# Kernel tuning notes

Hardware: AMD Instinct MI355X
Metric: run time of the kernel (lower is better)

## Reference

```python
import jax, jax.numpy as jnp
import numpy as np

N_USERS = 100000
N_ITEMS = 200000
N_NODES = N_USERS + N_ITEMS
EMB_DIM = 64
N_LAYERS = 3
NNZ = 4000000


def setup_inputs() -> dict:
    key = jax.random.key(0)
    k1, k2, k3, k4, k5 = jax.random.split(key, 5)
    # xavier_uniform bound for [n, d] embedding
    bu = float(np.sqrt(6.0 / (N_USERS + EMB_DIM)))
    bi = float(np.sqrt(6.0 / (N_ITEMS + EMB_DIM)))
    user_table = jax.random.uniform(k1, (N_USERS, EMB_DIM), jnp.float32, -bu, bu)
    item_table = jax.random.uniform(k2, (N_ITEMS, EMB_DIM), jnp.float32, -bi, bi)
    adj_rows = jax.random.randint(k3, (NNZ,), 0, N_NODES, dtype=jnp.int32)
    adj_cols = jax.random.randint(k4, (NNZ,), 0, N_NODES, dtype=jnp.int32)
    # symmetric-normalized adjacency values are small positive floats
    adj_vals = jax.random.uniform(k5, (NNZ,), jnp.float32) * 0.1
    return {"user_table": user_table, "item_table": item_table,
            "adj_rows": adj_rows, "adj_cols": adj_cols, "adj_vals": adj_vals}


def _spmm(rows, cols, vals, x):
    # out[r] = sum_{nnz with row r} vals * x[col]  (COO SpMM)
    msgs = vals[:, None] * x[cols]                      # [nnz, D]
    return jax.ops.segment_sum(msgs, rows, num_segments=N_NODES)


def reference(user_table, item_table, adj_rows, adj_cols, adj_vals):
    # forward(adj_norm, perturb=False) in eval mode (dropout inactive)
    emb = jnp.concatenate([user_table, item_table], axis=0)  # [N, D]
    acc = emb  # running sum over layer outputs (incl. layer 0)
    cur = emb
    for _ in range(N_LAYERS):
        cur = _spmm(adj_rows, adj_cols, adj_vals, cur)
        acc = acc + cur
    all_emb = acc / (N_LAYERS + 1)  # mean over stacked layer embeddings
    user_emb = all_emb[:N_USERS]
    item_emb = all_emb[N_USERS:]
    return (user_emb, item_emb)
```

## Files before the change

kernel.cpp:

```cpp
#include <hip/hip_runtime.h>

#define N_USERS 100000
#define N_ITEMS 200000
#define N_NODES (N_USERS + N_ITEMS)
#define EMB     64
#define NNZ     4000000

#define BSHIFT 10
#define BROWS  (1 << BSHIFT)
#define NBUCK  ((N_NODES + BROWS - 1) >> BSHIFT)

#define AGG_THR    512
#define AGG_EPT    8
#define AGG_T      (AGG_THR * AGG_EPT)
#define AGG_BLOCKS ((NNZ + AGG_T - 1) / AGG_T)
#define SCAN_N     512

#define SEGCAP 16384
#define PCAP   SEGCAP
#define PITER  (PCAP / 1024)

typedef _Float16 h4 __attribute__((ext_vector_type(4)));


__global__ __launch_bounds__(AGG_THR)
void bucket_agg_kernel(const int*   __restrict__ rows,
                       const int*   __restrict__ cols,
                       const float* __restrict__ vals,
                       int*         __restrict__ bcnt,
                       float2*      __restrict__ pay) {
    __shared__ int            cntS[SCAN_N];
    __shared__ int            hoff[SCAN_N];
    __shared__ float2         payS[AGG_T];
    __shared__ unsigned short bidS[AGG_T];

    int tid  = threadIdx.x;
    int base = blockIdx.x * AGG_T;

    for (int i = tid; i < SCAN_N; i += AGG_THR) cntS[i] = 0;
    __syncthreads();

    unsigned pk[AGG_EPT];
#pragma unroll
    for (int j = 0; j < AGG_EPT; j++) {
        int e = base + j * AGG_THR + tid;
        pk[j] = 0xFFFFFFFFu;
        if (e < NNZ) {
            int r  = rows[e];
            int b  = r >> BSHIFT;
            int lp = atomicAdd(&cntS[b], 1);
            pk[j]  = ((unsigned)b << 22) | ((unsigned)(r & (BROWS - 1)) << 12)
                   | (unsigned)lp;
        }
    }
    __syncthreads();

    int v = cntS[tid];
    for (int off = 1; off < SCAN_N; off <<= 1) {
        int t = 0;
        if (tid >= off) t = cntS[tid - off];
        __syncthreads();
        if (tid >= off) cntS[tid] += t;
        __syncthreads();
    }
    int excl = cntS[tid] - v;

    if (tid < NBUCK && v > 0) hoff[tid] = atomicAdd(&bcnt[tid * 16], v);
    __syncthreads();
    cntS[tid] = excl;
    __syncthreads();

#pragma unroll
    for (int j = 0; j < AGG_EPT; j++) {
        if (pk[j] != 0xFFFFFFFFu) {
            int e   = base + j * AGG_THR + tid;
            int b   = pk[j] >> 22;
            int rl  = (pk[j] >> 12) & (BROWS - 1);
            int lp  = pk[j] & 0xFFF;
            int idx = cntS[b] + lp;
            unsigned packed = (unsigned)cols[e] | ((unsigned)rl << 19);
            payS[idx] = make_float2(__uint_as_float(packed), vals[e]);
            bidS[idx] = (unsigned short)b;
        }
    }
    __syncthreads();

    int total = NNZ - base; if (total > AGG_T) total = AGG_T;
    for (int i = tid; i < total; i += AGG_THR) {
        int b   = bidS[i];
        int pos = hoff[b] + (i - cntS[b]);
        if (pos < SEGCAP)
            pay[(size_t)b * SEGCAP + pos] = payS[i];
    }
}

__global__ void bscan_kernel(const int* __restrict__ bcnt,
                             int* __restrict__ bbase,
                             int* __restrict__ row_ptr) {
    __shared__ int s[512];
    int tid = threadIdx.x;
    int v = 0;
    if (tid < NBUCK) {
        v = bcnt[tid * 16];
        if (v > SEGCAP) v = SEGCAP;
    }
    s[tid] = v;
    __syncthreads();
    for (int off = 1; off < 512; off <<= 1) {
        int t = 0;
        if (tid >= off) t = s[tid - off];
        __syncthreads();
        if (tid >= off) s[tid] += t;
        __syncthreads();
    }
    if (tid < NBUCK) bbase[tid] = s[tid] - v;
    if (tid == 511) bbase[NBUCK] = s[511];
    if (tid == 0)   row_ptr[N_NODES] = NNZ;
}

__global__ __launch_bounds__(1024)
void place_kernel(const int*    __restrict__ bcnt,
                  const int*    __restrict__ bbase,
                  const float2* __restrict__ pay,
                  int*          __restrict__ row_ptr,
                  float2*       __restrict__ edges) {
    __shared__ float2 payS[PCAP];
    __shared__ int    cntS[BROWS];
    int b   = blockIdx.x;
    int tid = threadIdx.x;
    int run = bcnt[b * 16]; if (run > PCAP) run = PCAP;
    int beg = bbase[b];
    const float2* seg = pay + (size_t)b * SEGCAP;

    cntS[tid] = 0;
    __syncthreads();

    unsigned eu[PITER]; float ev[PITER]; int elp[PITER];
#pragma unroll
    for (int j = 0; j < PITER; j++) {
        int i = j * 1024 + tid;
        eu[j] = 0xFFFFFFFFu;
        if (i < run) {
            float2 p = seg[i];
            unsigned u = __float_as_uint(p.x);
            eu[j] = u;
            ev[j] = p.y;
            elp[j] = atomicAdd(&cntS[(u >> 19) & (BROWS - 1)], 1);
        }
    }
    __syncthreads();

    for (int off = 1; off < BROWS; off <<= 1) {
        int t = 0;
        if (tid >= off) t = cntS[tid - off];
        __syncthreads();
        if (tid >= off) cntS[tid] += t;
        __syncthreads();
    }

    int gr = (b << BSHIFT) + tid;
    if (gr < N_NODES)
        row_ptr[gr] = beg + (tid ? cntS[tid - 1] : 0);

#pragma unroll
    for (int j = 0; j < PITER; j++) {
        if (eu[j] != 0xFFFFFFFFu) {
            int r    = (int)((eu[j] >> 19) & (BROWS - 1));
            int base = (r == 0) ? 0 : cntS[r - 1];
            payS[base + elp[j]] = make_float2(__uint_as_float(eu[j] & 0x7FFFFu), ev[j]);
        }
    }
    __syncthreads();

    for (int i = tid; i < run; i += 1024) {
        edges[beg + i] = payS[i];
    }
}

__global__ void initH_kernel(const float* __restrict__ user_t,
                             const float* __restrict__ item_t,
                             _Float16* __restrict__ eh) {
    int i = blockIdx.x * blockDim.x + threadIdx.x;
    const int total4 = N_NODES * EMB / 4;
    if (i >= total4) return;
    int fi   = i * 4;
    int node = fi >> 6;
    int off  = fi & 63;
    float4 v;
    if (node < N_USERS)
        v = *(const float4*)(user_t + (size_t)node * EMB + off);
    else
        v = *(const float4*)(item_t + (size_t)(node - N_USERS) * EMB + off);
    h4 h = { (_Float16)v.x, (_Float16)v.y, (_Float16)v.z, (_Float16)v.w };
    *(h4*)(eh + fi) = h;
}

__device__ __forceinline__ float4 row_gather_h(const int*      __restrict__ rp,
                                               const float2*   __restrict__ edges,
                                               const _Float16* __restrict__ xh,
                                               int row, int s) {
    int i   = rp[row];
    int end = rp[row + 1];
    float4 acc = make_float4(0.f, 0.f, 0.f, 0.f);
    for (; i + 3 < end; i += 4) {
        float2 e0 = edges[i];
        float2 e1 = edges[i + 1];
        float2 e2 = edges[i + 2];
        float2 e3 = edges[i + 3];
        h4 a = *(const h4*)(xh + ((size_t)__float_as_int(e0.x) << 6) + (s << 2));
        h4 b = *(const h4*)(xh + ((size_t)__float_as_int(e1.x) << 6) + (s << 2));
        h4 c = *(const h4*)(xh + ((size_t)__float_as_int(e2.x) << 6) + (s << 2));
        h4 d = *(const h4*)(xh + ((size_t)__float_as_int(e3.x) << 6) + (s << 2));
        acc.x += e0.y * (float)a.x + e1.y * (float)b.x + e2.y * (float)c.x + e3.y * (float)d.x;
        acc.y += e0.y * (float)a.y + e1.y * (float)b.y + e2.y * (float)c.y + e3.y * (float)d.y;
        acc.z += e0.y * (float)a.z + e1.y * (float)b.z + e2.y * (float)c.z + e3.y * (float)d.z;
        acc.w += e0.y * (float)a.w + e1.y * (float)b.w + e2.y * (float)c.w + e3.y * (float)d.w;
    }
    for (; i < end; ++i) {
        float2 e0 = edges[i];
        h4 a = *(const h4*)(xh + ((size_t)__float_as_int(e0.x) << 6) + (s << 2));
        acc.x += e0.y * (float)a.x;
        acc.y += e0.y * (float)a.y;
        acc.z += e0.y * (float)a.z;
        acc.w += e0.y * (float)a.w;
    }
    return acc;
}

__global__ void spmm_yh_kernel(const int*      __restrict__ rp,
                               const float2*   __restrict__ edges,
                               const _Float16* __restrict__ xh,
                               _Float16*       __restrict__ yh) {
    int t    = blockIdx.x * blockDim.x + threadIdx.x;
    int wid  = t >> 6;
    int lane = t & 63;
    int q    = lane >> 4;
    int s    = lane & 15;
    int row  = (wid << 2) + q;
    if (row >= N_NODES) return;
    float4 acc = row_gather_h(rp, edges, xh, row, s);
    h4 h = { (_Float16)acc.x, (_Float16)acc.y, (_Float16)acc.z, (_Float16)acc.w };
    *(h4*)(yh + (((size_t)row << 6) + (s << 2))) = h;
}

__global__ void spmm_fin_kernel(const int*      __restrict__ rp,
                                const float2*   __restrict__ edges,
                                const float*    __restrict__ user_t,
                                const float*    __restrict__ item_t,
                                const _Float16* __restrict__ y1h,
                                const _Float16* __restrict__ y2h,
                                float*          __restrict__ out) {
    int t    = blockIdx.x * blockDim.x + threadIdx.x;
    int wid  = t >> 6;
    int lane = t & 63;
    int q    = lane >> 4;
    int s    = lane & 15;
    int row  = (wid << 2) + q;
    if (row >= N_NODES) return;
    float4 acc = row_gather_h(rp, edges, y2h, row, s);
    size_t o = ((size_t)row << 6) + (s << 2);
    float4 ev;
    if (row < N_USERS)
        ev = *(const float4*)(user_t + o);
    else
        ev = *(const float4*)(item_t + o - ((size_t)N_USERS << 6));
    h4 v1 = *(const h4*)(y1h + o);
    h4 v2 = *(const h4*)(y2h + o);
    float4 r;
    r.x = (ev.x + (float)v1.x + (float)v2.x + acc.x) * 0.25f;
    r.y = (ev.y + (float)v1.y + (float)v2.y + acc.y) * 0.25f;
    r.z = (ev.z + (float)v1.z + (float)v2.z + acc.z) * 0.25f;
    r.w = (ev.w + (float)v1.w + (float)v2.w + acc.w) * 0.25f;
    *(float4*)(out + o) = r;
}

__global__ void init_kernel(const float* __restrict__ user_t,
                            const float* __restrict__ item_t,
                            float* __restrict__ out,
                            float* __restrict__ bufA,
                            float* __restrict__ bufB) {
    int i = blockIdx.x * blockDim.x + threadIdx.x;
    const int total4 = N_NODES * EMB / 4;
    if (i >= total4) return;
    int fi   = i * 4;
    int node = fi >> 6;
    int off  = fi & 63;
    float4 v;
    if (node < N_USERS)
        v = *(const float4*)(user_t + (size_t)node * EMB + off);
    else
        v = *(const float4*)(item_t + (size_t)(node - N_USERS) * EMB + off);
    *(float4*)(out  + fi) = v;
    *(float4*)(bufA + fi) = v;
    *(float4*)(bufB + fi) = make_float4(0.f, 0.f, 0.f, 0.f);
}

__global__ void spmm_kernel(const int*   __restrict__ rows,
                            const int*   __restrict__ cols,
                            const float* __restrict__ vals,
                            const float* __restrict__ x,
                            float*       __restrict__ y) {
    int tid  = blockIdx.x * blockDim.x + threadIdx.x;
    int e    = tid >> 6;
    int lane = tid & 63;
    if (e >= NNZ) return;
    atomicAdd(&y[(size_t)rows[e] * EMB + lane], vals[e] * x[(size_t)cols[e] * EMB + lane]);
}

__global__ void acc_zero_kernel(float* __restrict__ out,
                                const float* __restrict__ src,
                                float* __restrict__ zbuf) {
    int i = blockIdx.x * blockDim.x + threadIdx.x;
    const int total4 = N_NODES * EMB / 4;
    if (i >= total4) return;
    int fi = i * 4;
    float4 o = *(float4*)(out + fi);
    float4 s = *(const float4*)(src + fi);
    o.x += s.x; o.y += s.y; o.z += s.z; o.w += s.w;
    *(float4*)(out  + fi) = o;
    *(float4*)(zbuf + fi) = make_float4(0.f, 0.f, 0.f, 0.f);
}

__global__ void final_kernel(float* __restrict__ out,
                             const float* __restrict__ src) {
    int i = blockIdx.x * blockDim.x + threadIdx.x;
    const int total4 = N_NODES * EMB / 4;
    if (i >= total4) return;
    int fi = i * 4;
    float4 o = *(float4*)(out + fi);
    float4 s = *(const float4*)(src + fi);
    o.x = (o.x + s.x) * 0.25f;
    o.y = (o.y + s.y) * 0.25f;
    o.z = (o.z + s.z) * 0.25f;
    o.w = (o.w + s.w) * 0.25f;
    *(float4*)(out + fi) = o;
}

extern "C" void kernel_launch(void* const* d_in, const int* in_sizes, int n_in,
                              void* d_out, int out_size, void* d_ws, size_t ws_size,
                              hipStream_t stream) {
    const float* user_t = (const float*)d_in[0];
    const float* item_t = (const float*)d_in[1];
    const int*   rows   = (const int*)d_in[2];
    const int*   cols   = (const int*)d_in[3];
    const float* vals   = (const float*)d_in[4];
    float* out = (float*)d_out;

    const size_t embh_bytes = (size_t)N_NODES * EMB * 2;
    const size_t emb_bytes  = (size_t)N_NODES * EMB * 4;
    const size_t pay_bytes  = (size_t)NBUCK * SEGCAP * 8;
    const size_t r0_bytes   = (pay_bytes > embh_bytes ? pay_bytes : embh_bytes);
    const size_t edges_bytes = (size_t)NNZ * 8;
    const size_t small_bytes = (size_t)(N_NODES + 1) * 4
                             + (size_t)NBUCK * 16 * 4
                             + (size_t)(NBUCK + 1) * 4;
    const int total4    = N_NODES * EMB / 4;
    const int ew_blocks = (total4 + 255) / 256;

    const size_t need_h = r0_bytes + 2 * embh_bytes + edges_bytes + small_bytes;
    const int spmm_blocks = (int)(((size_t)N_NODES / 4 * 64 + 255) / 256);

    if (ws_size >= need_h) {
        char* p = (char*)d_ws;
        char*     region0 = p;           p += r0_bytes;
        _Float16* y1h     = (_Float16*)p; p += embh_bytes;
        _Float16* y2h     = (_Float16*)p; p += embh_bytes;
        float2*   edges   = (float2*)p;   p += edges_bytes;
        int*      row_ptr = (int*)p;      p += (size_t)(N_NODES + 1) * 4;
        int*      bcnt    = (int*)p;      p += (size_t)NBUCK * 16 * 4;
        int*      bbase   = (int*)p;
        float2*   pay = (float2*)region0;
        _Float16* eh  = (_Float16*)region0;

        hipMemsetAsync(bcnt, 0, (size_t)NBUCK * 16 * 4, stream);
        bucket_agg_kernel<<<AGG_BLOCKS, AGG_THR, 0, stream>>>(rows, cols, vals, bcnt, pay);
        bscan_kernel<<<1, 512, 0, stream>>>(bcnt, bbase, row_ptr);
        place_kernel<<<NBUCK, 1024, 0, stream>>>(bcnt, bbase, pay, row_ptr, edges);

        initH_kernel<<<ew_blocks, 256, 0, stream>>>(user_t, item_t, eh);

        spmm_yh_kernel <<<spmm_blocks, 256, 0, stream>>>(row_ptr, edges, eh,  y1h);
        spmm_yh_kernel <<<spmm_blocks, 256, 0, stream>>>(row_ptr, edges, y1h, y2h);
        spmm_fin_kernel<<<spmm_blocks, 256, 0, stream>>>(row_ptr, edges, user_t, item_t,
                                                         y1h, y2h, out);
    } else {
        char* p = (char*)d_ws;
        float* bufA = (float*)p; p += emb_bytes;
        float* bufB = (float*)p;
        const int spmmA_blocks = (int)(((size_t)NNZ * 64 + 255) / 256);
        init_kernel<<<ew_blocks, 256, 0, stream>>>(user_t, item_t, out, bufA, bufB);
        spmm_kernel<<<spmmA_blocks, 256, 0, stream>>>(rows, cols, vals, bufA, bufB);
        acc_zero_kernel<<<ew_blocks, 256, 0, stream>>>(out, bufB, bufA);
        spmm_kernel<<<spmmA_blocks, 256, 0, stream>>>(rows, cols, vals, bufB, bufA);
        acc_zero_kernel<<<ew_blocks, 256, 0, stream>>>(out, bufA, bufB);
        spmm_kernel<<<spmmA_blocks, 256, 0, stream>>>(rows, cols, vals, bufA, bufB);
        final_kernel<<<ew_blocks, 256, 0, stream>>>(out, bufB);
    }
}
```

Measured before the change: 511.6 us.

## Halve bucket size, use wave-shuffle scans, fuse fp16 embedding init into place kernel

Bucket width drops from 1024 to 512 rows, so there are about 586 buckets. The place kernel now runs 512 threads with half the shared memory, which should allow more blocks per CU. The shared-memory Hillis-Steele scans with a barrier per step are replaced by wave shuffle scans plus a cross-wave prefix, which cuts barrier count. The separate fp16 conversion kernel is folded into the place kernel, which removes a launch. In exchange the pay buffer and eh no longer alias, so more workspace is needed. The fused conversion uses scalar loads rather than float4, and the per-bucket capacity is halved to 8192, which would silently drop edges if a bucket overflowed (mean load is about 6.8k per bucket).

```diff
diff --git a/kernel.cpp b/kernel.cpp
--- a/kernel.cpp
+++ b/kernel.cpp
@@ -6,22 +6,30 @@
 #define EMB     64
 #define NNZ     4000000
 
-#define BSHIFT 10
+#define BSHIFT 9
 #define BROWS  (1 << BSHIFT)
 #define NBUCK  ((N_NODES + BROWS - 1) >> BSHIFT)
+#define NB2    1024
 
 #define AGG_THR    512
 #define AGG_EPT    8
 #define AGG_T      (AGG_THR * AGG_EPT)
 #define AGG_BLOCKS ((NNZ + AGG_T - 1) / AGG_T)
-#define SCAN_N     512
-
-#define SEGCAP 16384
-#define PCAP   SEGCAP
-#define PITER  (PCAP / 1024)
+
+#define SEGCAP 8192
+#define PITER  (SEGCAP / 512)
 
 typedef _Float16 h4 __attribute__((ext_vector_type(4)));
 
+
+__device__ __forceinline__ int wave_incl_scan(int v, int lane) {
+#pragma unroll
+    for (int d = 1; d < 64; d <<= 1) {
+        int t = __shfl_up(v, d, 64);
+        if (lane >= d) v += t;
+    }
+    return v;
+}
 
 __global__ __launch_bounds__(AGG_THR)
 void bucket_agg_kernel(const int*   __restrict__ rows,
@@ -29,15 +37,19 @@
                        const float* __restrict__ vals,
                        int*         __restrict__ bcnt,
                        float2*      __restrict__ pay) {
-    __shared__ int            cntS[SCAN_N];
-    __shared__ int            hoff[SCAN_N];
+    __shared__ int            cntS[NB2];
+    __shared__ int            hoff[NB2];
+    __shared__ int            waveTotS[8];
     __shared__ float2         payS[AGG_T];
     __shared__ unsigned short bidS[AGG_T];
 
     int tid  = threadIdx.x;
+    int lane = tid & 63;
+    int wid  = tid >> 6;
     int base = blockIdx.x * AGG_T;
 
-    for (int i = tid; i < SCAN_N; i += AGG_THR) cntS[i] = 0;
+    cntS[tid]       = 0;
+    cntS[tid + 512] = 0;
     __syncthreads();
 
     unsigned pk[AGG_EPT];
@@ -49,32 +61,34 @@
             int r  = rows[e];
             int b  = r >> BSHIFT;
             int lp = atomicAdd(&cntS[b], 1);
-            pk[j]  = ((unsigned)b << 22) | ((unsigned)(r & (BROWS - 1)) << 12)
+            pk[j]  = ((unsigned)b << 21) | ((unsigned)(r & (BROWS - 1)) << 12)
                    | (unsigned)lp;
         }
     }
     __syncthreads();
 
-    int v = cntS[tid];
-    for (int off = 1; off < SCAN_N; off <<= 1) {
-        int t = 0;
-        if (tid >= off) t = cntS[tid - off];
-        __syncthreads();
-        if (tid >= off) cntS[tid] += t;
-        __syncthreads();
-    }
-    int excl = cntS[tid] - v;
-
-    if (tid < NBUCK && v > 0) hoff[tid] = atomicAdd(&bcnt[tid * 16], v);
-    __syncthreads();
-    cntS[tid] = excl;
+    int v0 = cntS[2 * tid];
+    int v1 = cntS[2 * tid + 1];
+    int pv = v0 + v1;
+    int incl = wave_incl_scan(pv, lane);
+    if (lane == 63) waveTotS[wid] = incl;
+    __syncthreads();
+    int wbase = 0;
+    for (int w = 0; w < wid; w++) wbase += waveTotS[w];
+    int excl0 = wbase + incl - pv;
+    int excl1 = excl0 + v0;
+
+    if (2 * tid     < NBUCK && v0 > 0) hoff[2 * tid    ] = atomicAdd(&bcnt[(2 * tid    ) * 16], v0);
+    if (2 * tid + 1 < NBUCK && v1 > 0) hoff[2 * tid + 1] = atomicAdd(&bcnt[(2 * tid + 1) * 16], v1);
+    cntS[2 * tid]     = excl0;
+    cntS[2 * tid + 1] = excl1;
     __syncthreads();
 
 #pragma unroll
     for (int j = 0; j < AGG_EPT; j++) {
         if (pk[j] != 0xFFFFFFFFu) {
             int e   = base + j * AGG_THR + tid;
-            int b   = pk[j] >> 22;
+            int b   = pk[j] >> 21;
             int rl  = (pk[j] >> 12) & (BROWS - 1);
             int lp  = pk[j] & 0xFFF;
             int idx = cntS[b] + lp;
@@ -97,7 +111,7 @@
 __global__ void bscan_kernel(const int* __restrict__ bcnt,
                              int* __restrict__ bbase,
                              int* __restrict__ row_ptr) {
-    __shared__ int s[512];
+    __shared__ int s[1024];
     int tid = threadIdx.x;
     int v = 0;
     if (tid < NBUCK) {
@@ -106,7 +120,7 @@
     }
     s[tid] = v;
     __syncthreads();
-    for (int off = 1; off < 512; off <<= 1) {
+    for (int off = 1; off < 1024; off <<= 1) {
         int t = 0;
         if (tid >= off) t = s[tid - off];
         __syncthreads();
@@ -114,22 +128,28 @@
         __syncthreads();
     }
     if (tid < NBUCK) bbase[tid] = s[tid] - v;
-    if (tid == 511) bbase[NBUCK] = s[511];
-    if (tid == 0)   row_ptr[N_NODES] = NNZ;
-}
-
-__global__ __launch_bounds__(1024)
+    if (tid == 1023) bbase[NBUCK] = s[1023];
+    if (tid == 0)    row_ptr[N_NODES] = NNZ;
+}
+
+__global__ __launch_bounds__(512)
 void place_kernel(const int*    __restrict__ bcnt,
                   const int*    __restrict__ bbase,
                   const float2* __restrict__ pay,
                   int*          __restrict__ row_ptr,
-                  float2*       __restrict__ edges) {
-    __shared__ float2 payS[PCAP];
+                  float2*       __restrict__ edges,
+                  const float*  __restrict__ user_t,
+                  const float*  __restrict__ item_t,
+                  _Float16*     __restrict__ eh) {
+    __shared__ float2 payS[SEGCAP];
     __shared__ int    cntS[BROWS];
-    int b   = blockIdx.x;
-    int tid = threadIdx.x;
-    int run = bcnt[b * 16]; if (run > PCAP) run = PCAP;
-    int beg = bbase[b];
+    __shared__ int    waveTotS[8];
+    int b    = blockIdx.x;
+    int tid  = threadIdx.x;
+    int lane = tid & 63;
+    int wid  = tid >> 6;
+    int run  = bcnt[b * 16]; if (run > SEGCAP) run = SEGCAP;
+    int beg  = bbase[b];
     const float2* seg = pay + (size_t)b * SEGCAP;
 
     cntS[tid] = 0;
@@ -138,7 +158,7 @@
     unsigned eu[PITER]; float ev[PITER]; int elp[PITER];
 #pragma unroll
     for (int j = 0; j < PITER; j++) {
-        int i = j * 1024 + tid;
+        int i = j * 512 + tid;
         eu[j] = 0xFFFFFFFFu;
         if (i < run) {
             float2 p = seg[i];
@@ -150,17 +170,18 @@
     }
     __syncthreads();
 
-    for (int off = 1; off < BROWS; off <<= 1) {
-        int t = 0;
-        if (tid >= off) t = cntS[tid - off];
-        __syncthreads();
-        if (tid >= off) cntS[tid] += t;
-        __syncthreads();
-    }
+    int v = cntS[tid];
+    int incl = wave_incl_scan(v, lane);
+    if (lane == 63) waveTotS[wid] = incl;
+    __syncthreads();
+    int wbase = 0;
+    for (int w = 0; w < wid; w++) wbase += waveTotS[w];
+    incl += wbase;
+    cntS[tid] = incl;
 
     int gr = (b << BSHIFT) + tid;
-    if (gr < N_NODES)
-        row_ptr[gr] = beg + (tid ? cntS[tid - 1] : 0);
+    if (gr < N_NODES) row_ptr[gr] = beg + incl - v;
+    __syncthreads();
 
 #pragma unroll
     for (int j = 0; j < PITER; j++) {
@@ -172,27 +193,23 @@
     }
     __syncthreads();
 
-    for (int i = tid; i < run; i += 1024) {
+    for (int i = tid; i < run; i += 512) {
         edges[beg + i] = payS[i];
     }
-}
-
-__global__ void initH_kernel(const float* __restrict__ user_t,
-                             const float* __restrict__ item_t,
-                             _Float16* __restrict__ eh) {
-    int i = blockIdx.x * blockDim.x + threadIdx.x;
-    const int total4 = N_NODES * EMB / 4;
-    if (i >= total4) return;
-    int fi   = i * 4;
-    int node = fi >> 6;
-    int off  = fi & 63;
-    float4 v;
-    if (node < N_USERS)
-        v = *(const float4*)(user_t + (size_t)node * EMB + off);
-    else
-        v = *(const float4*)(item_t + (size_t)(node - N_USERS) * EMB + off);
-    h4 h = { (_Float16)v.x, (_Float16)v.y, (_Float16)v.z, (_Float16)v.w };
-    *(h4*)(eh + fi) = h;
+
+    int r0   = b << BSHIFT;
+    int nrow = N_NODES - r0; if (nrow > BROWS) nrow = BROWS;
+    if (nrow > 0) {
+        int nel = nrow << 6;
+        for (int i = tid; i < nel; i += 512) {
+            int gr2 = r0 + (i >> 6);
+            int d   = i & 63;
+            float x = (gr2 < N_USERS)
+                    ? user_t[(size_t)gr2 * EMB + d]
+                    : item_t[(size_t)(gr2 - N_USERS) * EMB + d];
+            eh[(size_t)r0 * EMB + i] = (_Float16)x;
+        }
+    }
 }
 
 __device__ __forceinline__ float4 row_gather_h(const int*      __restrict__ rp,
@@ -346,10 +363,9 @@
     const float* vals   = (const float*)d_in[4];
     float* out = (float*)d_out;
 
-    const size_t embh_bytes = (size_t)N_NODES * EMB * 2;
-    const size_t emb_bytes  = (size_t)N_NODES * EMB * 4;
-    const size_t pay_bytes  = (size_t)NBUCK * SEGCAP * 8;
-    const size_t r0_bytes   = (pay_bytes > embh_bytes ? pay_bytes : embh_bytes);
+    const size_t embh_bytes  = (size_t)N_NODES * EMB * 2;
+    const size_t emb_bytes   = (size_t)N_NODES * EMB * 4;
+    const size_t pay_bytes   = (size_t)NBUCK * SEGCAP * 8;
     const size_t edges_bytes = (size_t)NNZ * 8;
     const size_t small_bytes = (size_t)(N_NODES + 1) * 4
                              + (size_t)NBUCK * 16 * 4
@@ -357,27 +373,25 @@
     const int total4    = N_NODES * EMB / 4;
     const int ew_blocks = (total4 + 255) / 256;
 
-    const size_t need_h = r0_bytes + 2 * embh_bytes + edges_bytes + small_bytes;
+    const size_t need_h = pay_bytes + 3 * embh_bytes + edges_bytes + small_bytes;
     const int spmm_blocks = (int)(((size_t)N_NODES / 4 * 64 + 255) / 256);
 
     if (ws_size >= need_h) {
         char* p = (char*)d_ws;
-        char*     region0 = p;           p += r0_bytes;
+        float2*   pay     = (float2*)p;   p += pay_bytes;
+        _Float16* eh      = (_Float16*)p; p += embh_bytes;
         _Float16* y1h     = (_Float16*)p; p += embh_bytes;
         _Float16* y2h     = (_Float16*)p; p += embh_bytes;
         float2*   edges   = (float2*)p;   p += edges_bytes;
         int*      row_ptr = (int*)p;      p += (size_t)(N_NODES + 1) * 4;
         int*      bcnt    = (int*)p;      p += (size_t)NBUCK * 16 * 4;
         int*      bbase   = (int*)p;
-        float2*   pay = (float2*)region0;
-        _Float16* eh  = (_Float16*)region0;
 
         hipMemsetAsync(bcnt, 0, (size_t)NBUCK * 16 * 4, stream);
         bucket_agg_kernel<<<AGG_BLOCKS, AGG_THR, 0, stream>>>(rows, cols, vals, bcnt, pay);
-        bscan_kernel<<<1, 512, 0, stream>>>(bcnt, bbase, row_ptr);
-        place_kernel<<<NBUCK, 1024, 0, stream>>>(bcnt, bbase, pay, row_ptr, edges);
-
-        initH_kernel<<<ew_blocks, 256, 0, stream>>>(user_t, item_t, eh);
+        bscan_kernel<<<1, 1024, 0, stream>>>(bcnt, bbase, row_ptr);
+        place_kernel<<<NBUCK, 512, 0, stream>>>(bcnt, bbase, pay, row_ptr, edges,
+                                                user_t, item_t, eh);
 
         spmm_yh_kernel <<<spmm_blocks, 256, 0, stream>>>(row_ptr, edges, eh,  y1h);
         spmm_yh_kernel <<<spmm_blocks, 256, 0, stream>>>(row_ptr, edges, y1h, y2h);
```

Result: slower. 556.5 us (+8.8%).
